# Performance work log

Measured on AMD Instinct MI355X. Metric: run time of the kernel, lower is better.

Reference implementation:

```python
import jax, jax.numpy as jnp
import numpy as np

EPS = 1e-5

def setup_inputs() -> dict:
    key = jax.random.key(0)
    ks = jax.random.split(key, 10)
    B, N, D = 1, 20000, 256
    E, H = 320000, 8
    s = 1.0 / np.sqrt(D)
    return {
        "node_embeddings": jax.random.normal(ks[0], (B, N, D), jnp.float32),
        "edge_index": jax.random.randint(ks[1], (2, E), 0, N, jnp.int32),
        "edge_weights": jax.random.uniform(ks[2], (E,), jnp.float32),
        "Wq": jax.random.normal(ks[3], (D, D), jnp.float32) * s,
        "Wk": jax.random.normal(ks[4], (D, D), jnp.float32) * s,
        "Wv": jax.random.normal(ks[5], (D, D), jnp.float32) * s,
        "We": jax.random.normal(ks[6], (H,), jnp.float32),  # edge_encoder weight [num_heads,1] squeezed
        "Wo": jax.random.normal(ks[7], (D, D), jnp.float32) * s,
        "ln_g": jnp.ones((D,), jnp.float32),
        "ln_b": jnp.zeros((D,), jnp.float32),
    }

def reference(node_embeddings, edge_index, edge_weights, Wq, Wk, Wv, We, Wo, ln_g, ln_b):
    B, N, D = node_embeddings.shape
    H = We.shape[0]
    hd = D // H
    scale = 1.0 / np.sqrt(hd)
    residual = node_embeddings

    # projections -> [B, N, H, hd]
    Q = (node_embeddings @ Wq).reshape(B, N, H, hd)
    K = (node_embeddings @ Wk).reshape(B, N, H, hd)
    V = (node_embeddings @ Wv).reshape(B, N, H, hd)

    src = edge_index[0]
    tgt = edge_index[1]
    E = src.shape[0]

    # gather per edge, edge axis leading for segment ops: [E, B, H, hd]
    Q_e = jnp.moveaxis(Q[:, src], 1, 0)
    K_e = jnp.moveaxis(K[:, tgt], 1, 0)
    V_e = jnp.moveaxis(V[:, tgt], 1, 0)

    # per-edge scores [E, B, H]
    scores = (Q_e * K_e).sum(-1) * scale
    bias = edge_weights[:, None] * We[None, :]            # [E, H]
    scores = scores + bias[:, None, :]

    # scatter softmax grouped by source node
    m = jax.ops.segment_max(scores, src, num_segments=N)   # [N, B, H]
    p = jnp.exp(scores - m[src])
    denom = jax.ops.segment_sum(p, src, num_segments=N)    # [N, B, H]
    attn = p / denom[src]                                   # [E, B, H]

    # scatter-add weighted V -> [N, B, H, hd]
    weighted = attn[..., None] * V_e
    agg = jax.ops.segment_sum(weighted.reshape(E, -1), src, num_segments=N)
    agg = agg.reshape(N, B, H, hd)

    attn_out = jnp.moveaxis(agg, 0, 1).reshape(B, N, D)     # [B, N, D]
    out = attn_out @ Wo

    x = out + residual
    mu = x.mean(-1, keepdims=True)
    var = ((x - mu) ** 2).mean(-1, keepdims=True)
    return (x - mu) / jnp.sqrt(var + EPS) * ln_g + ln_b
```

## Files before the change

kernel.cpp:

```cpp
#include <hip/hip_runtime.h>
#include <hip/hip_bf16.h>

typedef __attribute__((ext_vector_type(8))) short short8;
typedef __attribute__((ext_vector_type(4))) short short4_t;
typedef __attribute__((ext_vector_type(4))) float f32x4;

#define CH 64

__device__ __forceinline__ ushort f2b(float f) {
  __hip_bfloat16 h = __float2bfloat16(f);
  return *reinterpret_cast<ushort*>(&h);
}
__device__ __forceinline__ float b2f(ushort u) {
  return __uint_as_float(((unsigned)u) << 16);
}
__device__ __forceinline__ void wave_lds_sync() {
  asm volatile("s_waitcnt lgkmcnt(0)" ::: "memory");
  __builtin_amdgcn_wave_barrier();
}

__global__ __launch_bounds__(256) void pre_kernel(
    const float* __restrict__ Wq, const float* __restrict__ Wk,
    const float* __restrict__ Wv, const float* __restrict__ Wo,
    ushort* __restrict__ Wt, int* __restrict__ counts, int N) {
  __shared__ float L[32][33];
  int b = blockIdx.x;
  int t = threadIdx.x;
  if (b < 256) {
    int mat = b >> 6;
    int tile = b & 63;
    int tr = (tile >> 3) * 32;
    int tc = (tile & 7) * 32;
    const float* W = (mat == 0) ? Wq : (mat == 1) ? Wk : (mat == 2) ? Wv : Wo;
    int c = t & 31, r8 = t >> 5;
#pragma unroll
    for (int rr = 0; rr < 4; ++rr) {
      int r = r8 + rr * 8;
      L[r][c] = W[(size_t)(tr + r) * 256 + tc + c];
    }
    __syncthreads();
#pragma unroll
    for (int rr = 0; rr < 4; ++rr) {
      int cc = r8 + rr * 8;
      Wt[(size_t)(mat * 256 + tc + cc) * 256 + tr + c] = f2b(L[c][cc]);
    }
  } else {
    int i = (b - 256) * 256 + t;
    if (i < N) counts[i] = 0;
  }
}

__global__ __launch_bounds__(256) void hist_gemm(
    const float* __restrict__ X, const ushort* __restrict__ Wt,
    ushort* __restrict__ QKVb, const int* __restrict__ src,
    int* __restrict__ counts, int N, int E, int ngemm) {
  __shared__ ushort sA[128 * 64];
  __shared__ ushort sB[128 * 64];
  int bid = blockIdx.x;
  int t = threadIdx.x;
  if (bid >= ngemm) {
    int e = (bid - ngemm) * 256 + t;
    if (e < E) atomicAdd(&counts[src[e]], 1);
    return;
  }
  int bx = bid / 6, by = bid % 6;
  char* cA = (char*)sA;
  char* cB = (char*)sB;
  int lane = t & 63, w = t >> 6;
  int wr = w >> 1, wc = w & 1;
  int row0 = bx * 128;
  int lr = lane & 15, kg = lane >> 4;
  f32x4 acc[4][4] = {};
  for (int k0 = 0; k0 < 256; k0 += 64) {
#pragma unroll
    for (int it = 0; it < 4; ++it) {
      int slot = t + it * 256;
      int row = slot >> 3, kc = slot & 7;
      int grow = min(row0 + row, N - 1);
      const float* xp = X + (size_t)grow * 256 + k0 + kc * 8;
      float4 x0 = *reinterpret_cast<const float4*>(xp);
      float4 x1 = *reinterpret_cast<const float4*>(xp + 4);
      short8 va;
      va[0] = (short)f2b(x0.x); va[1] = (short)f2b(x0.y);
      va[2] = (short)f2b(x0.z); va[3] = (short)f2b(x0.w);
      va[4] = (short)f2b(x1.x); va[5] = (short)f2b(x1.y);
      va[6] = (short)f2b(x1.z); va[7] = (short)f2b(x1.w);
      *reinterpret_cast<short8*>(cA + ((row * 128 + kc * 16) ^ ((row & 7) << 4))) = va;
      short8 vb = *reinterpret_cast<const short8*>(Wt + (size_t)(by * 128 + row) * 256 + k0 + kc * 8);
      *reinterpret_cast<short8*>(cB + ((row * 128 + kc * 16) ^ ((row & 7) << 4))) = vb;
    }
    __syncthreads();
#pragma unroll
    for (int ks = 0; ks < 2; ++ks) {
      short8 af[4], bf[4];
#pragma unroll
      for (int fr = 0; fr < 4; ++fr) {
        int row = wr * 64 + fr * 16 + lr;
        af[fr] = *reinterpret_cast<const short8*>(
            cA + ((row * 128 + ks * 64 + kg * 16) ^ ((row & 7) << 4)));
      }
#pragma unroll
      for (int fc = 0; fc < 4; ++fc) {
        int col = wc * 64 + fc * 16 + lr;
        bf[fc] = *reinterpret_cast<const short8*>(
            cB + ((col * 128 + ks * 64 + kg * 16) ^ ((col & 7) << 4)));
      }
#pragma unroll
      for (int fr = 0; fr < 4; ++fr)
#pragma unroll
        for (int fc = 0; fc < 4; ++fc)
          acc[fr][fc] = __builtin_amdgcn_mfma_f32_16x16x32_bf16(af[fr], bf[fc], acc[fr][fc], 0, 0, 0);
    }
    __syncthreads();
  }
  int orow = kg * 4;
#pragma unroll
  for (int fr = 0; fr < 4; ++fr)
#pragma unroll
    for (int fc = 0; fc < 4; ++fc)
#pragma unroll
      for (int r = 0; r < 4; ++r) {
        int row = row0 + wr * 64 + fr * 16 + orow + r;
        int col = by * 128 + wc * 64 + fc * 16 + lr;
        if (row < N) QKVb[(size_t)row * 768 + col] = f2b(acc[fr][fc][r]);
      }
}

__global__ __launch_bounds__(1024) void scan_kernel(
    const int* __restrict__ counts, int* __restrict__ offs, int* __restrict__ cursor, int N) {
  __shared__ int wsum[16];
  __shared__ int wexc[16];
  __shared__ int s_total;
  int t = threadIdx.x;
  int lane = t & 63, wv = t >> 6;
  int per = (N + 1023) >> 10;
  int b0 = t * per;
  int e0 = min(b0 + per, N);
  int sum = 0;
  for (int i = b0; i < e0; ++i) sum += counts[i];
  int x = sum;
#pragma unroll
  for (int off = 1; off < 64; off <<= 1) {
    int y = __shfl_up(x, off);
    if (lane >= off) x += y;
  }
  if (lane == 63) wsum[wv] = x;
  __syncthreads();
  if (t < 64) {
    int s = (lane < 16) ? wsum[lane] : 0;
    int xs = s;
#pragma unroll
    for (int off = 1; off < 16; off <<= 1) {
      int y = __shfl_up(xs, off);
      if (lane >= off) xs += y;
    }
    if (lane < 16) wexc[lane] = xs - s;
    if (lane == 15) s_total = xs;
  }
  __syncthreads();
  int running = wexc[wv] + (x - sum);
  for (int i = b0; i < e0; ++i) {
    int c = counts[i];
    offs[i] = running;
    cursor[i] = running;
    running += c;
  }
  if (t == 0) offs[N] = s_total;
}

__global__ void scatter_kernel(const int* __restrict__ src, const int* __restrict__ tgt,
                               const float* __restrict__ ew, int* __restrict__ cursor,
                               int* __restrict__ tgt_s, float* __restrict__ w_s, int E) {
  int e = blockIdx.x * blockDim.x + threadIdx.x;
  if (e < E) {
    int pos = atomicAdd(&cursor[src[e]], 1);
    tgt_s[pos] = tgt[e];
    w_s[pos] = ew[e];
  }
}

__global__ __launch_bounds__(256) void attn_kernel(
    const ushort* __restrict__ QKVb,
    const int* __restrict__ offs, const int* __restrict__ tgt_s, const float* __restrict__ w_s,
    const float* __restrict__ We, ushort* __restrict__ AGGb, int N) {
  __shared__ float s_p[4][CH][8];
  __shared__ int s_tgt[4][CH];
  __shared__ float s_w[4][CH];
  int t = threadIdx.x;
  int w = t >> 6;
  int l = t & 63;
  int i = blockIdx.x * 4 + w;
  if (i >= N) return;
  int e8 = l >> 3;
  int h = l & 7;
  int hacc = l >> 3;
  const float scale = 0.17677669529663687f;
  float we = We[h];

  float qf[32];
  {
    const short8* qr = reinterpret_cast<const short8*>(QKVb + (size_t)i * 768 + h * 32);
#pragma unroll
    for (int d = 0; d < 4; ++d) {
      short8 qv = qr[d];
#pragma unroll
      for (int x = 0; x < 8; ++x) qf[d * 8 + x] = b2f((ushort)qv[x]);
    }
  }

  float m = -1e30f, lsum = 0.f;
  float acc0 = 0.f, acc1 = 0.f, acc2 = 0.f, acc3 = 0.f;
  int beg = offs[i], end = offs[i + 1];

  for (int base = beg; base < end; base += CH) {
    int cnt = min(CH, end - base);
    int cnt_pad = (cnt + 7) & ~7;
    {
      bool valid = l < cnt;
      int tg = valid ? tgt_s[base + l] : i;
      float ww = valid ? w_s[base + l] : 0.f;
      s_tgt[w][l] = tg;
      s_w[w][l] = ww;
    }
    wave_lds_sync();

    __builtin_amdgcn_s_setprio(1);
    short8 kc[4], kn[4];
    {
      const short8* p = reinterpret_cast<const short8*>(
          QKVb + (size_t)s_tgt[w][e8] * 768 + 256 + h * 32);
#pragma unroll
      for (int d = 0; d < 4; ++d) kc[d] = p[d];
    }
    if (8 < cnt_pad) {
      const short8* p = reinterpret_cast<const short8*>(
          QKVb + (size_t)s_tgt[w][8 + e8] * 768 + 256 + h * 32);
#pragma unroll
      for (int d = 0; d < 4; ++d) kn[d] = p[d];
    }

    float s_local[8];
#pragma unroll
    for (int it = 0; it < 8; ++it) s_local[it] = -1e30f;
    float cmax = -1e30f;
#pragma unroll
    for (int it = 0; it < 8; ++it) {
      if (it * 8 >= cnt_pad) break;
      float dot = 0.f;
#pragma unroll
      for (int d = 0; d < 4; ++d)
#pragma unroll
        for (int x = 0; x < 8; ++x)
          dot += qf[d * 8 + x] * b2f((ushort)kc[d][x]);
      int j = it * 8 + e8;
      float s = (j < cnt) ? dot * scale + s_w[w][j] * we : -1e30f;
      s_local[it] = s;
      cmax = fmaxf(cmax, s);
#pragma unroll
      for (int d = 0; d < 4; ++d) kc[d] = kn[d];
      if ((it + 2) * 8 < cnt_pad) {
        const short8* p = reinterpret_cast<const short8*>(
            QKVb + (size_t)s_tgt[w][(it + 2) * 8 + e8] * 768 + 256 + h * 32);
#pragma unroll
        for (int d = 0; d < 4; ++d) kn[d] = p[d];
      }
    }

    short4_t vc[8], vn[8];
#pragma unroll
    for (int k = 0; k < 8; ++k)
      vc[k] = *reinterpret_cast<const short4_t*>(
          QKVb + (size_t)s_tgt[w][k] * 768 + 512 + l * 4);
    if (8 < cnt_pad) {
#pragma unroll
      for (int k = 0; k < 8; ++k)
        vn[k] = *reinterpret_cast<const short4_t*>(
            QKVb + (size_t)s_tgt[w][8 + k] * 768 + 512 + l * 4);
    }

    cmax = fmaxf(cmax, __shfl_xor(cmax, 8));
    cmax = fmaxf(cmax, __shfl_xor(cmax, 16));
    cmax = fmaxf(cmax, __shfl_xor(cmax, 32));
    float newm = fmaxf(m, cmax);
    float f = __expf(m - newm);
    float psum = 0.f;
#pragma unroll
    for (int it = 0; it < 8; ++it) {
      if (it * 8 >= cnt_pad) break;
      int j = it * 8 + e8;
      float p = __expf(s_local[it] - newm);
      s_p[w][j][h] = p;
      psum += p;
    }
    psum += __shfl_xor(psum, 8);
    psum += __shfl_xor(psum, 16);
    psum += __shfl_xor(psum, 32);
    lsum = lsum * f + psum;
    m = newm;
    float f_acc = __shfl(f, hacc);
    acc0 *= f_acc; acc1 *= f_acc; acc2 *= f_acc; acc3 *= f_acc;
    wave_lds_sync();

#pragma unroll
    for (int g = 0; g < 8; ++g) {
      if (g * 8 >= cnt_pad) break;
      float pv[8];
#pragma unroll
      for (int k = 0; k < 8; ++k) pv[k] = s_p[w][g * 8 + k][hacc];
#pragma unroll
      for (int k = 0; k < 8; ++k) {
        acc0 += pv[k] * b2f((ushort)vc[k][0]);
        acc1 += pv[k] * b2f((ushort)vc[k][1]);
        acc2 += pv[k] * b2f((ushort)vc[k][2]);
        acc3 += pv[k] * b2f((ushort)vc[k][3]);
      }
#pragma unroll
      for (int k = 0; k < 8; ++k) vc[k] = vn[k];
      if ((g + 2) * 8 < cnt_pad) {
#pragma unroll
        for (int k = 0; k < 8; ++k)
          vn[k] = *reinterpret_cast<const short4_t*>(
              QKVb + (size_t)s_tgt[w][(g + 2) * 8 + k] * 768 + 512 + l * 4);
      }
    }
    __builtin_amdgcn_s_setprio(0);
    wave_lds_sync();
  }
  float lsum_acc = __shfl(lsum, hacc);
  float rinv = (lsum_acc > 0.f) ? 1.f / lsum_acc : 0.f;
  short4_t o;
  o[0] = (short)f2b(acc0 * rinv);
  o[1] = (short)f2b(acc1 * rinv);
  o[2] = (short)f2b(acc2 * rinv);
  o[3] = (short)f2b(acc3 * rinv);
  *reinterpret_cast<short4_t*>(AGGb + (size_t)i * 256 + l * 4) = o;
}

__global__ __launch_bounds__(256) void out_ln(
    const ushort* __restrict__ AGGb, const ushort* __restrict__ Wot,
    const float* __restrict__ X, const float* __restrict__ g, const float* __restrict__ bb,
    float* __restrict__ out, int N) {
  __shared__ ushort sA[64 * 64];
  __shared__ ushort sB[256 * 64];
  char* cA = (char*)sA;
  char* cB = (char*)sB;
  int t = threadIdx.x;
  int lane = t & 63, w = t >> 6;
  int row0 = blockIdx.x * 64;
  int lr = lane & 15, kg = lane >> 4;
  f32x4 acc[16] = {};
  for (int k0 = 0; k0 < 256; k0 += 64) {
#pragma unroll
    for (int it = 0; it < 2; ++it) {
      int slot = t + it * 256;
      int row = slot >> 3, kc = slot & 7;
      int grow = min(row0 + row, N - 1);
      short8 va = *reinterpret_cast<const short8*>(AGGb + (size_t)grow * 256 + k0 + kc * 8);
      *reinterpret_cast<short8*>(cA + ((row * 128 + kc * 16) ^ ((row & 7) << 4))) = va;
    }
#pragma unroll
    for (int it = 0; it < 8; ++it) {
      int slot = t + it * 256;
      int col = slot >> 3, kc = slot & 7;
      short8 vb = *reinterpret_cast<const short8*>(Wot + (size_t)col * 256 + k0 + kc * 8);
      *reinterpret_cast<short8*>(cB + ((col * 128 + kc * 16) ^ ((col & 7) << 4))) = vb;
    }
    __syncthreads();
#pragma unroll
    for (int ks = 0; ks < 2; ++ks) {
      int arow = w * 16 + lr;
      short8 a = *reinterpret_cast<const short8*>(
          cA + ((arow * 128 + ks * 64 + kg * 16) ^ ((arow & 7) << 4)));
#pragma unroll
      for (int fc = 0; fc < 16; ++fc) {
        int col = fc * 16 + lr;
        short8 b = *reinterpret_cast<const short8*>(
            cB + ((col * 128 + ks * 64 + kg * 16) ^ ((col & 7) << 4)));
        acc[fc] = __builtin_amdgcn_mfma_f32_16x16x32_bf16(a, b, acc[fc], 0, 0, 0);
      }
    }
    __syncthreads();
  }
  float g16[16], b16[16];
#pragma unroll
  for (int fc = 0; fc < 16; ++fc) {
    g16[fc] = g[fc * 16 + lr];
    b16[fc] = bb[fc * 16 + lr];
  }
#pragma unroll
  for (int r = 0; r < 4; ++r) {
    int rowl = kg * 4 + r;
    int grow = row0 + w * 16 + rowl;
    int growc = min(grow, N - 1);
    float xv[16];
    float s = 0.f, ss = 0.f;
#pragma unroll
    for (int fc = 0; fc < 16; ++fc) {
      float v = acc[fc][r] + X[(size_t)growc * 256 + fc * 16 + lr];
      xv[fc] = v;
      s += v;
      ss += v * v;
    }
    s += __shfl_xor(s, 1);  ss += __shfl_xor(ss, 1);
    s += __shfl_xor(s, 2);  ss += __shfl_xor(ss, 2);
    s += __shfl_xor(s, 4);  ss += __shfl_xor(ss, 4);
    s += __shfl_xor(s, 8);  ss += __shfl_xor(ss, 8);
    float mu = s * (1.f / 256.f);
    float var = ss * (1.f / 256.f) - mu * mu;
    float rs = rsqrtf(var + 1e-5f);
    if (grow < N) {
#pragma unroll
      for (int fc = 0; fc < 16; ++fc)
        out[(size_t)grow * 256 + fc * 16 + lr] = (xv[fc] - mu) * rs * g16[fc] + b16[fc];
    }
  }
}

extern "C" void kernel_launch(void* const* d_in, const int* in_sizes, int n_in,
                              void* d_out, int out_size, void* d_ws, size_t ws_size,
                              hipStream_t stream) {
  const float* X  = (const float*)d_in[0];
  const int* eidx = (const int*)d_in[1];
  const float* ew = (const float*)d_in[2];
  const float* Wq = (const float*)d_in[3];
  const float* Wk = (const float*)d_in[4];
  const float* Wv = (const float*)d_in[5];
  const float* We = (const float*)d_in[6];
  const float* Wo = (const float*)d_in[7];
  const float* g  = (const float*)d_in[8];
  const float* b  = (const float*)d_in[9];
  int N = in_sizes[0] / 256;
  int E = in_sizes[1] / 2;
  const int* src = eidx;
  const int* tgt = eidx + E;
  float* out = (float*)d_out;

  char* w = (char*)d_ws;
  ushort* Wt   = (ushort*)w;  w += (size_t)1024 * 256 * 2;
  ushort* QKVb = (ushort*)w;  w += (size_t)N * 768 * 2;
  ushort* AGGb = (ushort*)w;  w += (size_t)N * 256 * 2;
  int* counts  = (int*)w;     w += (size_t)N * 4;
  int* offs    = (int*)w;     w += (size_t)(N + 1) * 4;
  int* cursor  = (int*)w;     w += (size_t)N * 4;
  int* tgt_s   = (int*)w;     w += (size_t)E * 4;
  float* w_s   = (float*)w;   w += (size_t)E * 4;
  const ushort* Wot = Wt + (size_t)768 * 256;

  int nzero = (N + 255) / 256;
  pre_kernel<<<256 + nzero, 256, 0, stream>>>(Wq, Wk, Wv, Wo, Wt, counts, N);

  int ngemm = ((N + 127) / 128) * 6;
  int nhist = (E + 255) / 256;
  hist_gemm<<<ngemm + nhist, 256, 0, stream>>>(X, Wt, QKVb, src, counts, N, E, ngemm);

  scan_kernel<<<1, 1024, 0, stream>>>(counts, offs, cursor, N);
  scatter_kernel<<<(E + 255) / 256, 256, 0, stream>>>(src, tgt, ew, cursor, tgt_s, w_s, E);
  attn_kernel<<<(N + 3) / 4, 256, 0, stream>>>(QKVb, offs, tgt_s, w_s, We, AGGb, N);
  out_ln<<<(N + 63) / 64, 256, 0, stream>>>(AGGb, Wot, X, g, b, out, N);
}
```

Baseline: 169.7 us.

## Restructure pre-pass kernels, pack edge arrays, simplify V loads in attention

The histogram moves into pre_kernel, with counts zeroed by a memset, and the prefix scan becomes an extra block of the QKV GEMM launch. This removes the standalone single-block scan kernel and one launch. The scatter now writes target and weight as one packed int2, so attention reads a single 8-byte record per edge. In the attention kernel, the V register double-buffering and the s_setprio hints are dropped in favour of plain per-group loads. The scan now runs on 256 threads instead of 1024, so that block may take longer, and the V loads are no longer prefetched ahead of use.

```diff
diff --git a/kernel.cpp b/kernel.cpp
--- a/kernel.cpp
+++ b/kernel.cpp
@@ -22,7 +22,8 @@
 __global__ __launch_bounds__(256) void pre_kernel(
     const float* __restrict__ Wq, const float* __restrict__ Wk,
     const float* __restrict__ Wv, const float* __restrict__ Wo,
-    ushort* __restrict__ Wt, int* __restrict__ counts, int N) {
+    ushort* __restrict__ Wt, const int* __restrict__ src,
+    int* __restrict__ counts, int E) {
   __shared__ float L[32][33];
   int b = blockIdx.x;
   int t = threadIdx.x;
@@ -45,22 +46,53 @@
       Wt[(size_t)(mat * 256 + tc + cc) * 256 + tr + c] = f2b(L[c][cc]);
     }
   } else {
-    int i = (b - 256) * 256 + t;
-    if (i < N) counts[i] = 0;
-  }
-}
-
-__global__ __launch_bounds__(256) void hist_gemm(
+    int e = (b - 256) * 256 + t;
+    if (e < E) atomicAdd(&counts[src[e]], 1);
+  }
+}
+
+__global__ __launch_bounds__(256) void gemm_scan(
     const float* __restrict__ X, const ushort* __restrict__ Wt,
-    ushort* __restrict__ QKVb, const int* __restrict__ src,
-    int* __restrict__ counts, int N, int E, int ngemm) {
+    ushort* __restrict__ QKVb, const int* __restrict__ counts,
+    int* __restrict__ offs, int* __restrict__ cursor,
+    int N, int ngemm) {
   __shared__ ushort sA[128 * 64];
   __shared__ ushort sB[128 * 64];
+  __shared__ int wsum[4];
+  __shared__ int wexc[4];
+  __shared__ int s_total;
   int bid = blockIdx.x;
   int t = threadIdx.x;
-  if (bid >= ngemm) {
-    int e = (bid - ngemm) * 256 + t;
-    if (e < E) atomicAdd(&counts[src[e]], 1);
+  if (bid == ngemm) {
+    int lane = t & 63, wv = t >> 6;
+    int per = (N + 255) >> 8;
+    int b0 = t * per;
+    int e0 = min(b0 + per, N);
+    int sum = 0;
+    for (int i = b0; i < e0; ++i) sum += counts[i];
+    int x = sum;
+#pragma unroll
+    for (int off = 1; off < 64; off <<= 1) {
+      int y = __shfl_up(x, off);
+      if (lane >= off) x += y;
+    }
+    if (lane == 63) wsum[wv] = x;
+    __syncthreads();
+    if (t == 0) {
+      int run = 0;
+#pragma unroll
+      for (int k = 0; k < 4; ++k) { wexc[k] = run; run += wsum[k]; }
+      s_total = run;
+    }
+    __syncthreads();
+    int running = wexc[wv] + (x - sum);
+    for (int i = b0; i < e0; ++i) {
+      int c = counts[i];
+      offs[i] = running;
+      cursor[i] = running;
+      running += c;
+    }
+    if (t == 0) offs[N] = s_total;
     return;
   }
   int bx = bid / 6, by = bid % 6;
@@ -126,62 +158,19 @@
       }
 }
 
-__global__ __launch_bounds__(1024) void scan_kernel(
-    const int* __restrict__ counts, int* __restrict__ offs, int* __restrict__ cursor, int N) {
-  __shared__ int wsum[16];
-  __shared__ int wexc[16];
-  __shared__ int s_total;
-  int t = threadIdx.x;
-  int lane = t & 63, wv = t >> 6;
-  int per = (N + 1023) >> 10;
-  int b0 = t * per;
-  int e0 = min(b0 + per, N);
-  int sum = 0;
-  for (int i = b0; i < e0; ++i) sum += counts[i];
-  int x = sum;
-#pragma unroll
-  for (int off = 1; off < 64; off <<= 1) {
-    int y = __shfl_up(x, off);
-    if (lane >= off) x += y;
-  }
-  if (lane == 63) wsum[wv] = x;
-  __syncthreads();
-  if (t < 64) {
-    int s = (lane < 16) ? wsum[lane] : 0;
-    int xs = s;
-#pragma unroll
-    for (int off = 1; off < 16; off <<= 1) {
-      int y = __shfl_up(xs, off);
-      if (lane >= off) xs += y;
-    }
-    if (lane < 16) wexc[lane] = xs - s;
-    if (lane == 15) s_total = xs;
-  }
-  __syncthreads();
-  int running = wexc[wv] + (x - sum);
-  for (int i = b0; i < e0; ++i) {
-    int c = counts[i];
-    offs[i] = running;
-    cursor[i] = running;
-    running += c;
-  }
-  if (t == 0) offs[N] = s_total;
-}
-
 __global__ void scatter_kernel(const int* __restrict__ src, const int* __restrict__ tgt,
                                const float* __restrict__ ew, int* __restrict__ cursor,
-                               int* __restrict__ tgt_s, float* __restrict__ w_s, int E) {
+                               int2* __restrict__ ews, int E) {
   int e = blockIdx.x * blockDim.x + threadIdx.x;
   if (e < E) {
     int pos = atomicAdd(&cursor[src[e]], 1);
-    tgt_s[pos] = tgt[e];
-    w_s[pos] = ew[e];
+    ews[pos] = make_int2(tgt[e], __float_as_int(ew[e]));
   }
 }
 
 __global__ __launch_bounds__(256) void attn_kernel(
     const ushort* __restrict__ QKVb,
-    const int* __restrict__ offs, const int* __restrict__ tgt_s, const float* __restrict__ w_s,
+    const int* __restrict__ offs, const int2* __restrict__ ews,
     const float* __restrict__ We, ushort* __restrict__ AGGb, int N) {
   __shared__ float s_p[4][CH][8];
   __shared__ int s_tgt[4][CH];
@@ -217,14 +206,16 @@
     int cnt_pad = (cnt + 7) & ~7;
     {
       bool valid = l < cnt;
-      int tg = valid ? tgt_s[base + l] : i;
-      float ww = valid ? w_s[base + l] : 0.f;
-      s_tgt[w][l] = tg;
-      s_w[w][l] = ww;
+      int2 te = valid ? ews[base + l] : make_int2(i, 0);
+      s_tgt[w][l] = te.x;
+      s_w[w][l] = valid ? __int_as_float(te.y) : 0.f;
     }
     wave_lds_sync();
 
-    __builtin_amdgcn_s_setprio(1);
+    float s_local[8];
+#pragma unroll
+    for (int it = 0; it < 8; ++it) s_local[it] = -1e30f;
+
     short8 kc[4], kn[4];
     {
       const short8* p = reinterpret_cast<const short8*>(
@@ -238,10 +229,6 @@
 #pragma unroll
       for (int d = 0; d < 4; ++d) kn[d] = p[d];
     }
-
-    float s_local[8];
-#pragma unroll
-    for (int it = 0; it < 8; ++it) s_local[it] = -1e30f;
     float cmax = -1e30f;
 #pragma unroll
     for (int it = 0; it < 8; ++it) {
@@ -265,19 +252,6 @@
         for (int d = 0; d < 4; ++d) kn[d] = p[d];
       }
     }
-
-    short4_t vc[8], vn[8];
-#pragma unroll
-    for (int k = 0; k < 8; ++k)
-      vc[k] = *reinterpret_cast<const short4_t*>(
-          QKVb + (size_t)s_tgt[w][k] * 768 + 512 + l * 4);
-    if (8 < cnt_pad) {
-#pragma unroll
-      for (int k = 0; k < 8; ++k)
-        vn[k] = *reinterpret_cast<const short4_t*>(
-            QKVb + (size_t)s_tgt[w][8 + k] * 768 + 512 + l * 4);
-    }
-
     cmax = fmaxf(cmax, __shfl_xor(cmax, 8));
     cmax = fmaxf(cmax, __shfl_xor(cmax, 16));
     cmax = fmaxf(cmax, __shfl_xor(cmax, 32));
@@ -305,25 +279,22 @@
     for (int g = 0; g < 8; ++g) {
       if (g * 8 >= cnt_pad) break;
       float pv[8];
-#pragma unroll
-      for (int k = 0; k < 8; ++k) pv[k] = s_p[w][g * 8 + k][hacc];
+      short4_t vv[8];
 #pragma unroll
       for (int k = 0; k < 8; ++k) {
-        acc0 += pv[k] * b2f((ushort)vc[k][0]);
-        acc1 += pv[k] * b2f((ushort)vc[k][1]);
-        acc2 += pv[k] * b2f((ushort)vc[k][2]);
-        acc3 += pv[k] * b2f((ushort)vc[k][3]);
-      }
-#pragma unroll
-      for (int k = 0; k < 8; ++k) vc[k] = vn[k];
-      if ((g + 2) * 8 < cnt_pad) {
-#pragma unroll
-        for (int k = 0; k < 8; ++k)
-          vn[k] = *reinterpret_cast<const short4_t*>(
-              QKVb + (size_t)s_tgt[w][(g + 2) * 8 + k] * 768 + 512 + l * 4);
-      }
-    }
-    __builtin_amdgcn_s_setprio(0);
+        int j = g * 8 + k;
+        pv[k] = s_p[w][j][hacc];
+        vv[k] = *reinterpret_cast<const short4_t*>(
+            QKVb + (size_t)s_tgt[w][j] * 768 + 512 + l * 4);
+      }
+#pragma unroll
+      for (int k = 0; k < 8; ++k) {
+        acc0 += pv[k] * b2f((ushort)vv[k][0]);
+        acc1 += pv[k] * b2f((ushort)vv[k][1]);
+        acc2 += pv[k] * b2f((ushort)vv[k][2]);
+        acc3 += pv[k] * b2f((ushort)vv[k][3]);
+      }
+    }
     wave_lds_sync();
   }
   float lsum_acc = __shfl(lsum, hacc);
@@ -442,19 +413,18 @@
   int* counts  = (int*)w;     w += (size_t)N * 4;
   int* offs    = (int*)w;     w += (size_t)(N + 1) * 4;
   int* cursor  = (int*)w;     w += (size_t)N * 4;
-  int* tgt_s   = (int*)w;     w += (size_t)E * 4;
-  float* w_s   = (float*)w;   w += (size_t)E * 4;
+  int2* ews    = (int2*)w;    w += (size_t)E * 8;
   const ushort* Wot = Wt + (size_t)768 * 256;
 
-  int nzero = (N + 255) / 256;
-  pre_kernel<<<256 + nzero, 256, 0, stream>>>(Wq, Wk, Wv, Wo, Wt, counts, N);
+  hipMemsetAsync(counts, 0, (size_t)N * 4, stream);
+
+  int nhist = (E + 255) / 256;
+  pre_kernel<<<256 + nhist, 256, 0, stream>>>(Wq, Wk, Wv, Wo, Wt, src, counts, E);
 
   int ngemm = ((N + 127) / 128) * 6;
-  int nhist = (E + 255) / 256;
-  hist_gemm<<<ngemm + nhist, 256, 0, stream>>>(X, Wt, QKVb, src, counts, N, E, ngemm);
-
-  scan_kernel<<<1, 1024, 0, stream>>>(counts, offs, cursor, N);
-  scatter_kernel<<<(E + 255) / 256, 256, 0, stream>>>(src, tgt, ew, cursor, tgt_s, w_s, E);
-  attn_kernel<<<(N + 3) / 4, 256, 0, stream>>>(QKVb, offs, tgt_s, w_s, We, AGGb, N);
+  gemm_scan<<<ngemm + 1, 256, 0, stream>>>(X, Wt, QKVb, counts, offs, cursor, N, ngemm);
+
+  scatter_kernel<<<(E + 255) / 256, 256, 0, stream>>>(src, tgt, ew, cursor, ews, E);
+  attn_kernel<<<(N + 3) / 4, 256, 0, stream>>>(QKVb, offs, ews, We, AGGb, N);
   out_ln<<<(N + 63) / 64, 256, 0, stream>>>(AGGb, Wot, X, g, b, out, N);
 }
```

Result: no change. 172.7 us (+1.8%).
